# Kernel tuning notes

Hardware: AMD Instinct MI355X
Metric: run time of the kernel (lower is better)

Reference implementation:

```python
import jax, jax.numpy as jnp
import numpy as np

N = 50000   # nodes
E = 800000  # edges
C = 64      # num_channels
EPS = 1e-5


def setup_inputs() -> dict:
    key = jax.random.key(0)
    ks = jax.random.split(key, 12)
    x = jax.random.normal(ks[0], (N, C), dtype=jnp.float32)
    vec = jax.random.normal(ks[1], (N, 3, C), dtype=jnp.float32)
    senders = jax.random.randint(ks[2], (E,), 0, N, dtype=jnp.int32)
    receivers = jax.random.randint(ks[3], (E,), 0, N, dtype=jnp.int32)
    interaction_matrices = jax.random.normal(ks[4], (E, 3, 3), dtype=jnp.float32)
    # learned parameters
    ln_scale = jnp.ones((C,), dtype=jnp.float32)
    ln_bias = jnp.zeros((C,), dtype=jnp.float32)
    vln_weight = jnp.ones((C,), dtype=jnp.float32)  # VecLayerNorm weight (norm_type='none' -> identity norm, channel scale)
    w1 = jax.random.normal(ks[5], (C, 2 * C), dtype=jnp.float32) / np.sqrt(C)
    b1 = jnp.zeros((2 * C,), dtype=jnp.float32)
    w2 = jax.random.normal(ks[6], (2 * C, C), dtype=jnp.float32) / np.sqrt(2 * C)
    b2 = jnp.zeros((C,), dtype=jnp.float32)
    return {
        "x": x, "vec": vec, "senders": senders, "receivers": receivers,
        "interaction_matrices": interaction_matrices,
        "ln_scale": ln_scale, "ln_bias": ln_bias, "vln_weight": vln_weight,
        "w1": w1, "b1": b1, "w2": w2, "b2": b2,
    }


def reference(x, vec, senders, receivers, interaction_matrices,
              ln_scale, ln_bias, vln_weight, w1, b1, w2, b2):
    # LayerNorm(eps=1e-5) over channel dim
    mean = jnp.mean(x, axis=-1, keepdims=True)
    var = jnp.var(x, axis=-1, keepdims=True)
    x_norm = (x - mean) * jax.lax.rsqrt(var + EPS) * ln_scale + ln_bias
    # VecLayerNorm with norm_type='none': identity norm, learned per-channel weight
    vec_norm = vec * vln_weight  # [N, 3, C]
    # MLP: Dense(2C) -> silu -> Dense(C)
    p = jax.nn.silu(x_norm @ w1 + b1) @ w2 + b2  # [N, C]
    # gather to edges
    p_i = p[receivers]            # [E, C]
    p_j = p[senders]              # [E, C]
    vec_i = vec_norm[receivers]   # [E, 3, C]
    vec_j = vec_norm[senders]     # [E, 3, C]
    source_dipole = p_j[:, None, :] * vec_j                              # [E, 3, C]
    field_at_i = jnp.einsum('eij,ejc->eic', interaction_matrices, source_dipole)  # [E, 3, C]
    dEnergy = jnp.sum(p_i[:, None, :] * vec_i * field_at_i, axis=1)      # [E, C]
    dx = jax.ops.segment_sum(dEnergy, receivers, num_segments=x.shape[0])  # [N, C]
    return dx
```

## Files before the change

kernel.cpp:

```cpp
#include <hip/hip_runtime.h>

#define C 64
#define EPS 1e-5f
#define BUCK_CAP 1536
#define OVF_CAP 65536
#define SMASK 0x03ffffffu

typedef __attribute__((ext_vector_type(8))) short bf16x8;
typedef __attribute__((ext_vector_type(4))) float f32x4;

static __device__ __forceinline__ unsigned int f2bf(float f) {
  unsigned int x = __float_as_uint(f);
  return (x + 0x7fffu + ((x >> 16) & 1u)) >> 16;
}
static __device__ __forceinline__ float bflo2f(unsigned int p) {
  return __uint_as_float(p << 16);
}
static __device__ __forceinline__ float bfhi2f(unsigned int p) {
  return __uint_as_float(p & 0xffff0000u);
}

__global__ __launch_bounds__(256) void prep_weights(
    const float* __restrict__ w1, const float* __restrict__ w2,
    unsigned short* __restrict__ w1T, unsigned short* __restrict__ w2T) {
  int idx = blockIdx.x * 256 + threadIdx.x;
  if (idx < 2 * C * C) {
    int k = idx >> 6, c = idx & 63;
    w1T[idx] = (unsigned short)f2bf(w1[c * 2 * C + k]);
  } else if (idx < 4 * C * C) {
    int j = idx - 2 * C * C;
    int c = j >> 7, k = j & 127;
    w2T[j] = (unsigned short)f2bf(w2[k * C + c]);
  }
}

__global__ __launch_bounds__(256) void bin_kernel(
    const int* __restrict__ recv, const int* __restrict__ send,
    uint2* __restrict__ region, int* __restrict__ bucketCnt,
    int* __restrict__ ovfList, int* __restrict__ ovfCnt,
    int n_edges, int nbuck) {
  __shared__ int hist[1024];
  int t = threadIdx.x;
  for (int i = t; i < 1024; i += 256) hist[i] = 0;
  __syncthreads();

  int base = blockIdx.x * 4096;
  int myrecv[16], mysend[16];
#pragma unroll 16
  for (int j = 0; j < 16; j++) {
    int e = base + j * 256 + t;
    if (e < n_edges) {
      int r = recv[e];
      myrecv[j] = r;
      mysend[j] = send[e];
      atomicAdd(&hist[r >> 6], 1);
    } else {
      myrecv[j] = -1;
      mysend[j] = 0;
    }
  }
  __syncthreads();

  for (int i = t; i < nbuck; i += 256) {
    int c = hist[i];
    hist[i] = (c > 0) ? atomicAdd(&bucketCnt[i], c) : 0;
  }
  __syncthreads();

#pragma unroll 16
  for (int j = 0; j < 16; j++) {
    int r = myrecv[j];
    if (r >= 0) {
      int e = base + j * 256 + t;
      int b = r >> 6;
      int pos = atomicAdd(&hist[b], 1);
      if (pos < BUCK_CAP) {
        uint2 rec;
        rec.x = (unsigned)mysend[j] | ((unsigned)(r & 63) << 26);
        rec.y = (unsigned)e;
        region[(size_t)b * BUCK_CAP + pos] = rec;
      } else {
        int o = atomicAdd(ovfCnt, 1);
        if (o < OVF_CAP) ovfList[o] = e;
      }
    }
  }
}

__global__ __launch_bounds__(1024) void scan_buckets(
    const int* __restrict__ bucketCnt, int* __restrict__ bucketBase,
    int nbuck) {
  __shared__ int part[1024];
  int t = threadIdx.x;
  int v = 0;
  if (t < nbuck) {
    v = bucketCnt[t];
    if (v > BUCK_CAP) v = BUCK_CAP;
  }
  part[t] = v;
  __syncthreads();
  for (int d = 1; d < 1024; d <<= 1) {
    int u = (t >= d) ? part[t - d] : 0;
    __syncthreads();
    part[t] += u;
    __syncthreads();
  }
  bucketBase[t] = part[t] - v;
}

__global__ __launch_bounds__(256) void sort_kernel(
    const uint2* __restrict__ region, const int* __restrict__ bucketCnt,
    const int* __restrict__ bucketBase, const float* __restrict__ Mmat,
    uint2* __restrict__ fat, int* __restrict__ nodeBeg,
    int* __restrict__ nodeEnd, int n_nodes) {
  __shared__ uint2 buf[BUCK_CAP];
  __shared__ int hist[64];
  __shared__ int off[64];
  int b = blockIdx.x;
  int t = threadIdx.x;
  int cnt = bucketCnt[b];
  if (cnt > BUCK_CAP) cnt = BUCK_CAP;
  const uint2* reg = region + (size_t)b * BUCK_CAP;
  int base = bucketBase[b];

  if (t < 64) hist[t] = 0;
  __syncthreads();
  for (int i = t; i < cnt; i += 256) {
    uint2 r = reg[i];
    buf[i] = r;
    atomicAdd(&hist[r.x >> 26], 1);
  }
  __syncthreads();
  if (t == 0) {
    int run = 0;
#pragma unroll
    for (int j = 0; j < 64; j++) { off[j] = run; run += hist[j]; }
  }
  __syncthreads();
  for (int i = t; i < cnt; i += 256) {
    uint2 r = buf[i];
    int pos = atomicAdd(&off[r.x >> 26], 1);
    const float* Mp = Mmat + (size_t)r.y * 9;
    float m0 = Mp[0], m1 = Mp[1], m2 = Mp[2], m3 = Mp[3], m4 = Mp[4];
    float m5 = Mp[5], m6 = Mp[6], m7 = Mp[7], m8 = Mp[8];
    size_t fi = (size_t)(base + pos) * 3;
    uint2 wa, wb, wc;
    wa.x = r.x;
    wa.y = f2bf(m0) | (f2bf(m1) << 16);
    wb.x = f2bf(m2) | (f2bf(m3) << 16);
    wb.y = f2bf(m4) | (f2bf(m5) << 16);
    wc.x = f2bf(m6) | (f2bf(m7) << 16);
    wc.y = f2bf(m8);
    fat[fi] = wa;
    fat[fi + 1] = wb;
    fat[fi + 2] = wc;
  }
  __syncthreads();
  if (t < 64) {
    int node = b * 64 + t;
    if (node < n_nodes) {
      int end = off[t];
      nodeBeg[node] = base + (end - hist[t]);
      nodeEnd[node] = base + end;
    }
  }
}

__global__ __launch_bounds__(256, 4) void node_kernel(
    const float* __restrict__ x, const float* __restrict__ vec,
    const float* __restrict__ ln_scale, const float* __restrict__ ln_bias,
    const float* __restrict__ vln_w,
    const unsigned short* __restrict__ w1T, const float* __restrict__ b1,
    const unsigned short* __restrict__ w2T, const float* __restrict__ b2,
    uint2* __restrict__ D16, int n_nodes) {
  __shared__ unsigned short An[64 * 72];
  __shared__ unsigned short Ss[64 * 136];

  const int t = threadIdx.x;
  const int lane = t & 63;
  const int wave = t >> 6;
  const int l15 = lane & 15;
  const int q = lane >> 4;

  {
    int rowl = t >> 2;
    int part = t & 3;
    int node = blockIdx.x * 64 + rowl;
    int nc = node < n_nodes ? node : n_nodes - 1;
    const float* xp = x + (size_t)nc * C + part * 16;
    float xv[16];
    float s = 0.f;
#pragma unroll
    for (int i = 0; i < 4; i++) {
      float4 v = *(const float4*)(xp + i * 4);
      xv[i * 4 + 0] = v.x; xv[i * 4 + 1] = v.y;
      xv[i * 4 + 2] = v.z; xv[i * 4 + 3] = v.w;
      s += v.x + v.y + v.z + v.w;
    }
    s += __shfl_xor(s, 1);
    s += __shfl_xor(s, 2);
    float mean = s * (1.f / C);
    float vs = 0.f;
#pragma unroll
    for (int i = 0; i < 16; i++) {
      float d = xv[i] - mean;
      vs += d * d;
    }
    vs += __shfl_xor(vs, 1);
    vs += __shfl_xor(vs, 2);
    float rs = rsqrtf(vs * (1.f / C) + EPS);
    float ls[16], lb[16];
#pragma unroll
    for (int i = 0; i < 4; i++) {
      float4 a = *(const float4*)(ln_scale + part * 16 + i * 4);
      float4 b = *(const float4*)(ln_bias + part * 16 + i * 4);
      ls[i * 4 + 0] = a.x; ls[i * 4 + 1] = a.y; ls[i * 4 + 2] = a.z; ls[i * 4 + 3] = a.w;
      lb[i * 4 + 0] = b.x; lb[i * 4 + 1] = b.y; lb[i * 4 + 2] = b.z; lb[i * 4 + 3] = b.w;
    }
    unsigned int bp[8];
#pragma unroll
    for (int i = 0; i < 8; i++) {
      float e0 = (xv[2 * i] - mean) * rs * ls[2 * i] + lb[2 * i];
      float e1 = (xv[2 * i + 1] - mean) * rs * ls[2 * i + 1] + lb[2 * i + 1];
      bp[i] = f2bf(e0) | (f2bf(e1) << 16);
    }
    uint4* dst = (uint4*)(An + rowl * 72 + part * 16);
    uint4 p0 = {bp[0], bp[1], bp[2], bp[3]};
    uint4 p1 = {bp[4], bp[5], bp[6], bp[7]};
    dst[0] = p0;
    dst[1] = p1;
  }
  __syncthreads();

  const int Mbase = wave * 16;

  bf16x8 a0 = *(const bf16x8*)(An + (Mbase + l15) * 72 + q * 8);
  bf16x8 a1 = *(const bf16x8*)(An + (Mbase + l15) * 72 + 32 + q * 8);
  f32x4 acc1[8];
#pragma unroll
  for (int nt = 0; nt < 8; nt++) {
    const unsigned short* wb = w1T + (nt * 16 + l15) * 64 + q * 8;
    bf16x8 b0 = *(const bf16x8*)(wb);
    bf16x8 b1f = *(const bf16x8*)(wb + 32);
    f32x4 z = {0.f, 0.f, 0.f, 0.f};
    z = __builtin_amdgcn_mfma_f32_16x16x32_bf16(a0, b0, z, 0, 0, 0);
    z = __builtin_amdgcn_mfma_f32_16x16x32_bf16(a1, b1f, z, 0, 0, 0);
    acc1[nt] = z;
  }
#pragma unroll
  for (int nt = 0; nt < 8; nt++) {
    float bb = b1[nt * 16 + l15];
#pragma unroll
    for (int r = 0; r < 4; r++) {
      float h = acc1[nt][r] + bb;
      float sg = h / (1.f + __expf(-h));
      Ss[(Mbase + q * 4 + r) * 136 + nt * 16 + l15] = (unsigned short)f2bf(sg);
    }
  }
  __syncthreads();

  bf16x8 a2[4];
#pragma unroll
  for (int kt = 0; kt < 4; kt++)
    a2[kt] = *(const bf16x8*)(Ss + (Mbase + l15) * 136 + kt * 32 + q * 8);
  f32x4 acc2[4];
#pragma unroll
  for (int nt = 0; nt < 4; nt++) {
    f32x4 z = {0.f, 0.f, 0.f, 0.f};
#pragma unroll
    for (int kt = 0; kt < 4; kt++) {
      bf16x8 b = *(const bf16x8*)(w2T + (nt * 16 + l15) * 128 + kt * 32 + q * 8);
      z = __builtin_amdgcn_mfma_f32_16x16x32_bf16(a2[kt], b, z, 0, 0, 0);
    }
    acc2[nt] = z;
  }

#pragma unroll
  for (int nt = 0; nt < 4; nt++) {
    int cc = nt * 16 + l15;
    float bb = b2[cc];
    float vw = vln_w[cc];
#pragma unroll
    for (int r = 0; r < 4; r++) {
      int rl = Mbase + q * 4 + r;
      int nn = blockIdx.x * 64 + rl;
      if (nn < n_nodes) {
        float p = (acc2[nt][r] + bb) * vw;
        const float* vp = vec + (size_t)nn * (3 * C) + cc;
        float v0 = vp[0], v1 = vp[C], v2 = vp[2 * C];
        uint2 u;
        u.x = f2bf(p * v0) | (f2bf(p * v1) << 16);
        u.y = f2bf(p * v2);
        D16[(size_t)nn * C + cc] = u;
      }
    }
  }
}

__global__ __launch_bounds__(256) void accum_node(
    const uint2* __restrict__ fat, const int* __restrict__ nodeBeg,
    const int* __restrict__ nodeEnd, const uint2* __restrict__ D2,
    float* __restrict__ dx, int n_nodes) {
  int wid = threadIdx.x >> 6;
  int lane = threadIdx.x & 63;
  int n = blockIdx.x * 4 + wid;
  if (n >= n_nodes) return;

  int beg = __builtin_amdgcn_readfirstlane(nodeBeg[n]);
  int end = __builtin_amdgcn_readfirstlane(nodeEnd[n]);

  uint2 dr = D2[(size_t)n * C + lane];
  float r0 = bflo2f(dr.x), r1 = bfhi2f(dr.x), r2 = bflo2f(dr.y);
  float acc = 0.f;

  if (beg < end) {
    const int last = end - 1;
    uint2 svA, svB, svC, svD, svE, svF, svG, svH;
    uint2 fA[3], fB[3], fC[3], fD[3], fE[3], fF[3], fG[3], fH[3];

#define LOADSLOT(SV, FM, IDX)                                                \
  {                                                                          \
    size_t fi_ = (size_t)(IDX) * 3;                                          \
    FM[0] = fat[fi_];                                                        \
    FM[1] = fat[fi_ + 1];                                                    \
    FM[2] = fat[fi_ + 2];                                                    \
    SV = D2[(size_t)(FM[0].x & SMASK) * C + lane];                           \
  }

#define COMPUTE(SV, FM)                                                      \
  {                                                                          \
    float a0 = bflo2f(SV.x), a1 = bfhi2f(SV.x), a2 = bflo2f(SV.y);           \
    float m00 = bflo2f(FM[0].y), m01 = bfhi2f(FM[0].y);                      \
    float m02 = bflo2f(FM[1].x), m10 = bfhi2f(FM[1].x);                      \
    float m11 = bflo2f(FM[1].y), m12 = bfhi2f(FM[1].y);                      \
    float m20 = bflo2f(FM[2].x), m21 = bfhi2f(FM[2].x);                      \
    float m22 = bflo2f(FM[2].y);                                             \
    float f0 = m00 * a0 + m01 * a1 + m02 * a2;                               \
    float f1 = m10 * a0 + m11 * a1 + m12 * a2;                               \
    float f2 = m20 * a0 + m21 * a1 + m22 * a2;                               \
    acc += r0 * f0 + r1 * f1 + r2 * f2;                                      \
  }

    int i1 = (beg + 1 > last) ? last : beg + 1;
    int i2 = (beg + 2 > last) ? last : beg + 2;
    int i3 = (beg + 3 > last) ? last : beg + 3;
    int i4 = (beg + 4 > last) ? last : beg + 4;
    int i5 = (beg + 5 > last) ? last : beg + 5;
    int i6 = (beg + 6 > last) ? last : beg + 6;
    int i7 = (beg + 7 > last) ? last : beg + 7;
    LOADSLOT(svA, fA, beg)
    LOADSLOT(svB, fB, i1)
    LOADSLOT(svC, fC, i2)
    LOADSLOT(svD, fD, i3)
    LOADSLOT(svE, fE, i4)
    LOADSLOT(svF, fF, i5)
    LOADSLOT(svG, fG, i6)
    LOADSLOT(svH, fH, i7)

    for (int e = beg; e <= last; e += 8) {
#define STAGE(K, SV, FM)                                                     \
  if (e + (K) <= last) {                                                     \
    COMPUTE(SV, FM)                                                          \
    int nx = e + (K) + 8;                                                    \
    if (nx <= last) LOADSLOT(SV, FM, nx)                                     \
  }
      STAGE(0, svA, fA)
      STAGE(1, svB, fB)
      STAGE(2, svC, fC)
      STAGE(3, svD, fD)
      STAGE(4, svE, fE)
      STAGE(5, svF, fF)
      STAGE(6, svG, fG)
      STAGE(7, svH, fH)
#undef STAGE
    }
#undef LOADSLOT
#undef COMPUTE
  }
  dx[(size_t)n * C + lane] = acc;
}

__global__ __launch_bounds__(256) void fixup_kernel(
    const int* __restrict__ ovfList, const int* __restrict__ ovfCnt,
    const int* __restrict__ senders, const int* __restrict__ receivers,
    const float* __restrict__ Mmat, const uint2* __restrict__ D2,
    float* __restrict__ dx) {
  int nov = *ovfCnt;
  if (nov > OVF_CAP) nov = OVF_CAP;
  int lane = threadIdx.x & 63;
  for (int idx = blockIdx.x * 4 + (threadIdx.x >> 6); idx < nov;
       idx += gridDim.x * 4) {
    int e = ovfList[idx];
    int s = senders[e];
    int r = receivers[e];
    uint2 sv = D2[(size_t)s * C + lane];
    uint2 rv = D2[(size_t)r * C + lane];
    const float* M = Mmat + (size_t)e * 9;
    float a0 = bflo2f(sv.x), a1 = bfhi2f(sv.x), a2 = bflo2f(sv.y);
    float c0 = bflo2f(rv.x), c1 = bfhi2f(rv.x), c2 = bflo2f(rv.y);
    float f0 = M[0] * a0 + M[1] * a1 + M[2] * a2;
    float f1 = M[3] * a0 + M[4] * a1 + M[5] * a2;
    float f2 = M[6] * a0 + M[7] * a1 + M[8] * a2;
    float dE = c0 * f0 + c1 * f1 + c2 * f2;
    atomicAdd(dx + (size_t)r * C + lane, dE);
  }
}

extern "C" void kernel_launch(void* const* d_in, const int* in_sizes, int n_in,
                              void* d_out, int out_size, void* d_ws, size_t ws_size,
                              hipStream_t stream) {
  const float* x        = (const float*)d_in[0];
  const float* vec      = (const float*)d_in[1];
  const int*   senders  = (const int*)d_in[2];
  const int*   receivers= (const int*)d_in[3];
  const float* Mmat     = (const float*)d_in[4];
  const float* ln_scale = (const float*)d_in[5];
  const float* ln_bias  = (const float*)d_in[6];
  const float* vln_w    = (const float*)d_in[7];
  const float* w1       = (const float*)d_in[8];
  const float* b1       = (const float*)d_in[9];
  const float* w2       = (const float*)d_in[10];
  const float* b2       = (const float*)d_in[11];
  float* dx = (float*)d_out;

  int n_nodes = in_sizes[0] / C;
  int n_edges = in_sizes[2];
  int nbuck = (n_nodes + 63) >> 6;

  unsigned short* w1T = (unsigned short*)d_ws;
  unsigned short* w2T = w1T + 2 * C * C;
  uint2* D16 = (uint2*)((char*)d_ws + 32768);
  char* p = (char*)d_ws + 32768 + (size_t)n_nodes * C * sizeof(uint2);
  p = (char*)(((size_t)p + 255) & ~(size_t)255);
  int* cnts       = (int*)p;  p += (1024 + 1) * 4;
  p = (char*)(((size_t)p + 255) & ~(size_t)255);
  int* bucketBase = (int*)p;  p += 1024 * 4;
  p = (char*)(((size_t)p + 255) & ~(size_t)255);
  uint2* region = (uint2*)p;  p += (size_t)nbuck * BUCK_CAP * 8;
  uint2* fat    = (uint2*)p;  p += (size_t)n_edges * 24;
  int* nodeBeg  = (int*)p;    p += (size_t)n_nodes * 4;
  int* nodeEnd  = (int*)p;    p += (size_t)n_nodes * 4;
  int* ovfList  = (int*)p;
  int* bucketCnt = cnts;
  int* ovfCnt = cnts + 1024;

  prep_weights<<<64, 256, 0, stream>>>(w1, w2, w1T, w2T);

  hipMemsetAsync(cnts, 0, (1024 + 1) * sizeof(int), stream);
  bin_kernel<<<(n_edges + 4095) / 4096, 256, 0, stream>>>(
      receivers, senders, region, bucketCnt, ovfList, ovfCnt, n_edges, nbuck);

  scan_buckets<<<1, 1024, 0, stream>>>(bucketCnt, bucketBase, nbuck);

  sort_kernel<<<nbuck, 256, 0, stream>>>(
      region, bucketCnt, bucketBase, Mmat, fat, nodeBeg, nodeEnd, n_nodes);

  node_kernel<<<(n_nodes + 63) / 64, 256, 0, stream>>>(
      x, vec, ln_scale, ln_bias, vln_w, w1T, b1, w2T, b2, D16, n_nodes);

  accum_node<<<(n_nodes + 3) / 4, 256, 0, stream>>>(
      fat, nodeBeg, nodeEnd, D16, dx, n_nodes);

  fixup_kernel<<<128, 256, 0, stream>>>(
      ovfList, ovfCnt, senders, receivers, Mmat, D16, dx);
}
```

Measured before the change: 269.8 us.

## Pack interaction matrices during binning, sort in place, drop scan and memset

Measured after the change: 272.2 us. About the same (+0.9%).

```diff
diff --git a/kernel.cpp b/kernel.cpp
--- a/kernel.cpp
+++ b/kernel.cpp
@@ -22,8 +22,10 @@
 
 __global__ __launch_bounds__(256) void prep_weights(
     const float* __restrict__ w1, const float* __restrict__ w2,
-    unsigned short* __restrict__ w1T, unsigned short* __restrict__ w2T) {
+    unsigned short* __restrict__ w1T, unsigned short* __restrict__ w2T,
+    int* __restrict__ cnts) {
   int idx = blockIdx.x * 256 + threadIdx.x;
+  if (idx < 1024 + 1) cnts[idx] = 0;
   if (idx < 2 * C * C) {
     int k = idx >> 6, c = idx & 63;
     w1T[idx] = (unsigned short)f2bf(w1[c * 2 * C + k]);
@@ -36,27 +38,25 @@
 
 __global__ __launch_bounds__(256) void bin_kernel(
     const int* __restrict__ recv, const int* __restrict__ send,
-    uint2* __restrict__ region, int* __restrict__ bucketCnt,
-    int* __restrict__ ovfList, int* __restrict__ ovfCnt,
-    int n_edges, int nbuck) {
+    const float* __restrict__ Mmat, uint2* __restrict__ fat,
+    int* __restrict__ bucketCnt, int* __restrict__ ovfList,
+    int* __restrict__ ovfCnt, int n_edges, int nbuck) {
   __shared__ int hist[1024];
   int t = threadIdx.x;
   for (int i = t; i < 1024; i += 256) hist[i] = 0;
   __syncthreads();
 
   int base = blockIdx.x * 4096;
-  int myrecv[16], mysend[16];
+  int myrecv[16];
 #pragma unroll 16
   for (int j = 0; j < 16; j++) {
     int e = base + j * 256 + t;
     if (e < n_edges) {
       int r = recv[e];
       myrecv[j] = r;
-      mysend[j] = send[e];
       atomicAdd(&hist[r >> 6], 1);
     } else {
       myrecv[j] = -1;
-      mysend[j] = 0;
     }
   }
   __syncthreads();
@@ -75,10 +75,20 @@
       int b = r >> 6;
       int pos = atomicAdd(&hist[b], 1);
       if (pos < BUCK_CAP) {
-        uint2 rec;
-        rec.x = (unsigned)mysend[j] | ((unsigned)(r & 63) << 26);
-        rec.y = (unsigned)e;
-        region[(size_t)b * BUCK_CAP + pos] = rec;
+        const float* Mp = Mmat + (size_t)e * 9;
+        float m0 = Mp[0], m1 = Mp[1], m2 = Mp[2], m3 = Mp[3], m4 = Mp[4];
+        float m5 = Mp[5], m6 = Mp[6], m7 = Mp[7], m8 = Mp[8];
+        size_t fi = (size_t)(b * BUCK_CAP + pos) * 3;
+        uint2 wa, wb, wc;
+        wa.x = (unsigned)send[e] | ((unsigned)(r & 63) << 26);
+        wa.y = f2bf(m0) | (f2bf(m1) << 16);
+        wb.x = f2bf(m2) | (f2bf(m3) << 16);
+        wb.y = f2bf(m4) | (f2bf(m5) << 16);
+        wc.x = f2bf(m6) | (f2bf(m7) << 16);
+        wc.y = f2bf(m8);
+        fat[fi] = wa;
+        fat[fi + 1] = wb;
+        fat[fi + 2] = wc;
       } else {
         int o = atomicAdd(ovfCnt, 1);
         if (o < OVF_CAP) ovfList[o] = e;
@@ -87,48 +97,26 @@
   }
 }
 
-__global__ __launch_bounds__(1024) void scan_buckets(
-    const int* __restrict__ bucketCnt, int* __restrict__ bucketBase,
-    int nbuck) {
-  __shared__ int part[1024];
-  int t = threadIdx.x;
-  int v = 0;
-  if (t < nbuck) {
-    v = bucketCnt[t];
-    if (v > BUCK_CAP) v = BUCK_CAP;
-  }
-  part[t] = v;
-  __syncthreads();
-  for (int d = 1; d < 1024; d <<= 1) {
-    int u = (t >= d) ? part[t - d] : 0;
-    __syncthreads();
-    part[t] += u;
-    __syncthreads();
-  }
-  bucketBase[t] = part[t] - v;
-}
-
 __global__ __launch_bounds__(256) void sort_kernel(
-    const uint2* __restrict__ region, const int* __restrict__ bucketCnt,
-    const int* __restrict__ bucketBase, const float* __restrict__ Mmat,
-    uint2* __restrict__ fat, int* __restrict__ nodeBeg,
-    int* __restrict__ nodeEnd, int n_nodes) {
-  __shared__ uint2 buf[BUCK_CAP];
+    uint2* __restrict__ fat, const int* __restrict__ bucketCnt,
+    int* __restrict__ nodeBeg, int* __restrict__ nodeEnd, int n_nodes) {
+  __shared__ uint2 buf[BUCK_CAP * 3];
   __shared__ int hist[64];
   __shared__ int off[64];
   int b = blockIdx.x;
   int t = threadIdx.x;
   int cnt = bucketCnt[b];
   if (cnt > BUCK_CAP) cnt = BUCK_CAP;
-  const uint2* reg = region + (size_t)b * BUCK_CAP;
-  int base = bucketBase[b];
+  uint2* fb = fat + (size_t)b * BUCK_CAP * 3;
 
   if (t < 64) hist[t] = 0;
   __syncthreads();
   for (int i = t; i < cnt; i += 256) {
-    uint2 r = reg[i];
-    buf[i] = r;
-    atomicAdd(&hist[r.x >> 26], 1);
+    uint2 r0 = fb[i * 3];
+    buf[i * 3] = r0;
+    buf[i * 3 + 1] = fb[i * 3 + 1];
+    buf[i * 3 + 2] = fb[i * 3 + 2];
+    atomicAdd(&hist[r0.x >> 26], 1);
   }
   __syncthreads();
   if (t == 0) {
@@ -138,30 +126,19 @@
   }
   __syncthreads();
   for (int i = t; i < cnt; i += 256) {
-    uint2 r = buf[i];
-    int pos = atomicAdd(&off[r.x >> 26], 1);
-    const float* Mp = Mmat + (size_t)r.y * 9;
-    float m0 = Mp[0], m1 = Mp[1], m2 = Mp[2], m3 = Mp[3], m4 = Mp[4];
-    float m5 = Mp[5], m6 = Mp[6], m7 = Mp[7], m8 = Mp[8];
-    size_t fi = (size_t)(base + pos) * 3;
-    uint2 wa, wb, wc;
-    wa.x = r.x;
-    wa.y = f2bf(m0) | (f2bf(m1) << 16);
-    wb.x = f2bf(m2) | (f2bf(m3) << 16);
-    wb.y = f2bf(m4) | (f2bf(m5) << 16);
-    wc.x = f2bf(m6) | (f2bf(m7) << 16);
-    wc.y = f2bf(m8);
-    fat[fi] = wa;
-    fat[fi + 1] = wb;
-    fat[fi + 2] = wc;
+    uint2 r0 = buf[i * 3];
+    int pos = atomicAdd(&off[r0.x >> 26], 1);
+    fb[pos * 3] = r0;
+    fb[pos * 3 + 1] = buf[i * 3 + 1];
+    fb[pos * 3 + 2] = buf[i * 3 + 2];
   }
   __syncthreads();
   if (t < 64) {
     int node = b * 64 + t;
     if (node < n_nodes) {
       int end = off[t];
-      nodeBeg[node] = base + (end - hist[t]);
-      nodeEnd[node] = base + end;
+      nodeBeg[node] = b * BUCK_CAP + (end - hist[t]);
+      nodeEnd[node] = b * BUCK_CAP + end;
     }
   }
 }
@@ -432,28 +409,23 @@
   uint2* D16 = (uint2*)((char*)d_ws + 32768);
   char* p = (char*)d_ws + 32768 + (size_t)n_nodes * C * sizeof(uint2);
   p = (char*)(((size_t)p + 255) & ~(size_t)255);
-  int* cnts       = (int*)p;  p += (1024 + 1) * 4;
+  int* cnts    = (int*)p;  p += (1024 + 1) * 4;
   p = (char*)(((size_t)p + 255) & ~(size_t)255);
-  int* bucketBase = (int*)p;  p += 1024 * 4;
-  p = (char*)(((size_t)p + 255) & ~(size_t)255);
-  uint2* region = (uint2*)p;  p += (size_t)nbuck * BUCK_CAP * 8;
-  uint2* fat    = (uint2*)p;  p += (size_t)n_edges * 24;
-  int* nodeBeg  = (int*)p;    p += (size_t)n_nodes * 4;
-  int* nodeEnd  = (int*)p;    p += (size_t)n_nodes * 4;
-  int* ovfList  = (int*)p;
+  uint2* fat   = (uint2*)p;  p += (size_t)nbuck * BUCK_CAP * 24;
+  int* nodeBeg = (int*)p;    p += (size_t)n_nodes * 4;
+  int* nodeEnd = (int*)p;    p += (size_t)n_nodes * 4;
+  int* ovfList = (int*)p;
   int* bucketCnt = cnts;
   int* ovfCnt = cnts + 1024;
 
-  prep_weights<<<64, 256, 0, stream>>>(w1, w2, w1T, w2T);
-
-  hipMemsetAsync(cnts, 0, (1024 + 1) * sizeof(int), stream);
+  prep_weights<<<64, 256, 0, stream>>>(w1, w2, w1T, w2T, cnts);
+
   bin_kernel<<<(n_edges + 4095) / 4096, 256, 0, stream>>>(
-      receivers, senders, region, bucketCnt, ovfList, ovfCnt, n_edges, nbuck);
-
-  scan_buckets<<<1, 1024, 0, stream>>>(bucketCnt, bucketBase, nbuck);
+      receivers, senders, Mmat, fat, bucketCnt, ovfList, ovfCnt,
+      n_edges, nbuck);
 
   sort_kernel<<<nbuck, 256, 0, stream>>>(
-      region, bucketCnt, bucketBase, Mmat, fat, nodeBeg, nodeEnd, n_nodes);
+      fat, bucketCnt, nodeBeg, nodeEnd, n_nodes);
 
   node_kernel<<<(n_nodes + 63) / 64, 256, 0, stream>>>(
       x, vec, ln_scale, ln_bias, vln_w, w1T, b1, w2T, b2, D16, n_nodes);
```
